# Kernel optimization log

Hardware: AMD Instinct MI355X
Metric: run time of the kernel (lower is better)

The kernel has to match this reference:

```python
import jax, jax.numpy as jnp
import numpy as np

NU = 50000   # num user nodes
NI = 50000   # num item nodes
E = 1600000  # edges per relation
DIN = 256    # in_features
H = 8        # n_heads
F = 64       # out_features per head (hidden = H*F = 512)
NEG_SLOPE = 0.2


def setup_inputs() -> dict:
    key = jax.random.key(0)
    ks = jax.random.split(key, 14)
    wscale = 0.05
    return {
        "x_user": jax.random.normal(ks[0], (NU, DIN), jnp.float32),
        "x_item": jax.random.normal(ks[1], (NI, DIN), jnp.float32),
        "Wv": jax.random.normal(ks[2], (3, DIN, H * F), jnp.float32) * wscale,
        "bv": jax.random.normal(ks[3], (3, H * F), jnp.float32) * wscale,
        "Wq": jax.random.normal(ks[4], (3, H * F, H), jnp.float32) * wscale,
        "bq": jax.random.normal(ks[5], (3, H), jnp.float32) * wscale,
        "Wk": jax.random.normal(ks[6], (3, H * F, H), jnp.float32) * wscale,
        "bk": jax.random.normal(ks[7], (3, H), jnp.float32) * wscale,
        "src1": jax.random.randint(ks[8], (E,), 0, NU, jnp.int32),   # user -> item
        "dst1": jax.random.randint(ks[9], (E,), 0, NI, jnp.int32),
        "src2": jax.random.randint(ks[10], (E,), 0, NI, jnp.int32),  # item -> user
        "dst2": jax.random.randint(ks[11], (E,), 0, NU, jnp.int32),
        "src3": jax.random.randint(ks[12], (E,), 0, NU, jnp.int32),  # user -> user
        "dst3": jax.random.randint(ks[13], (E,), 0, NU, jnp.int32),
    }


def _gat_relation(x_src, x_dst, Wv, bv, Wq, bq, Wk, bk, src, dst, n_dst):
    # linear_v on src and dst node features: [N, H*F]
    h_src = x_src @ Wv + bv
    h_dst = x_dst @ Wv + bv
    q = h_dst @ Wq + bq  # [Nd, H] per-head query logit
    k = h_src @ Wk + bk  # [Ns, H] per-head key logit
    # fused_gsddmm: gather to edges, leaky_relu, segment softmax over dst
    e = jax.nn.leaky_relu(q[dst] + k[src], NEG_SLOPE)  # [E, H]
    m = jax.ops.segment_max(e, dst, num_segments=n_dst)  # [Nd, H]
    m = jnp.where(jnp.isfinite(m), m, jnp.zeros_like(m))
    ex = jnp.exp(e - m[dst])
    denom = jax.ops.segment_sum(ex, dst, num_segments=n_dst)  # [Nd, H]
    attn = ex / jnp.maximum(denom[dst], 1e-9)  # [E, H]
    # gspmm: attention-weighted scatter-sum of src features into dst
    hs = h_src.reshape(-1, H, F)  # [Ns, H, F]
    agg = jax.ops.segment_sum(attn[:, :, None] * hs[src], dst, num_segments=n_dst)  # [Nd, H, F]
    return agg.mean(axis=1)  # torch.mean(h, dim=1) -> [Nd, F]


def reference(x_user, x_item, Wv, bv, Wq, bq, Wk, bk, src1, dst1, src2, dst2, src3, dst3):
    # relation 0: user -> item
    out_item = _gat_relation(x_user, x_item, Wv[0], bv[0], Wq[0], bq[0], Wk[0], bk[0], src1, dst1, NI)
    # relations 1 (item -> user) and 2 (user -> user) both target user: mean over relations
    r1 = _gat_relation(x_item, x_user, Wv[1], bv[1], Wq[1], bq[1], Wk[1], bk[1], src2, dst2, NU)
    r2 = _gat_relation(x_user, x_user, Wv[2], bv[2], Wq[2], bq[2], Wk[2], bk[2], src3, dst3, NU)
    out_user = (r1 + r2) / 2.0
    return out_user, out_item
```

## Files before the change

### kernel.cpp

```cpp
#include <hip/hip_runtime.h>

typedef unsigned short u16;
typedef __attribute__((ext_vector_type(4))) float f32x4;
typedef __attribute__((ext_vector_type(8))) short s16x8;

#define NND 50000
#define EDG 1600000
#define NBK 391
#define TOTB (3 * NBK)
#define TS 4096
#define CAPB 5120

__device__ __forceinline__ u16 f2b(float f) {
  union { float f; unsigned u; } c; c.f = f;
  unsigned r = c.u + 0x7fff + ((c.u >> 16) & 1);
  return (u16)(r >> 16);
}

__device__ __forceinline__ void accum8(float* num, uint4 u, float4 w0, float4 w1) {
  num[0] += w0.x * __int_as_float((int)(u.x << 16));
  num[1] += w0.y * __int_as_float((int)(u.x & 0xFFFF0000u));
  num[2] += w0.z * __int_as_float((int)(u.y << 16));
  num[3] += w0.w * __int_as_float((int)(u.y & 0xFFFF0000u));
  num[4] += w1.x * __int_as_float((int)(u.z << 16));
  num[5] += w1.y * __int_as_float((int)(u.z & 0xFFFF0000u));
  num[6] += w1.z * __int_as_float((int)(u.w << 16));
  num[7] += w1.w * __int_as_float((int)(u.w & 0xFFFF0000u));
}

__global__ void k_initcur(int* __restrict__ bcur) {
  int i = blockIdx.x * 256 + threadIdx.x;
  if (i < TOTB) bcur[i] = i * CAPB;
}

__global__ void k_prepw(const float* __restrict__ Wv, u16* __restrict__ Wt) {
  int tid = blockIdx.x * 256 + threadIdx.x;
  if (tid < 3 * 512 * 256) {
    int r = tid / (512 * 256); int rem = tid - r * 512 * 256;
    int n = rem >> 8; int kk = rem & 255;
    Wt[tid] = f2b(Wv[((size_t)r * 256 + kk) * 512 + n]);
  }
}

__global__ void k_fusew(const float* __restrict__ Wv, const float* __restrict__ bv,
                        const float* __restrict__ Wq, const float* __restrict__ bq,
                        const float* __restrict__ Wk, const float* __restrict__ bk,
                        float* __restrict__ FW, float* __restrict__ FB) {
  int tid = blockIdx.x * 256 + threadIdx.x;
  if (tid < 3 * 16 * 256) {
    int r = tid >> 12, o = (tid >> 8) & 15, kk = tid & 255;
    const float* wv = Wv + ((size_t)r * 256 + kk) * 512;
    const float* wqk = (o < 8) ? (Wq + r * 512 * 8 + o) : (Wk + r * 512 * 8 + (o - 8));
    float s = 0.f;
    for (int j = 0; j < 512; j++) s += wv[j] * wqk[j * 8];
    FW[tid] = s;
  }
  if (tid < 48) {
    int r = tid / 16, o = tid % 16;
    const float* wqk = (o < 8) ? (Wq + r * 512 * 8 + o) : (Wk + r * 512 * 8 + (o - 8));
    const float* bvp = bv + r * 512;
    float s = (o < 8) ? bq[r * 8 + o] : bk[r * 8 + (o - 8)];
    for (int j = 0; j < 512; j++) s += bvp[j] * wqk[j * 8];
    FB[tid] = s;
  }
}

__global__ void __launch_bounds__(256) kb_scatter(
    const int* __restrict__ s1, const int* __restrict__ d1,
    const int* __restrict__ s2, const int* __restrict__ d2,
    const int* __restrict__ s3, const int* __restrict__ d3,
    int* __restrict__ BCUR, unsigned* __restrict__ pairs) {
  __shared__ int h[NBK];
  __shared__ int bbase[NBK];
  int tid = threadIdx.x;
  int r = blockIdx.y;
  const int* dp = (r == 0) ? d1 : (r == 1) ? d2 : d3;
  const int* sp = (r == 0) ? s1 : (r == 1) ? s2 : s3;
  int e0 = blockIdx.x * TS;
  int n = EDG - e0; if (n > TS) n = TS;
  for (int b = tid; b < NBK; b += 256) h[b] = 0;
  __syncthreads();
  int eb[16]; unsigned ev[16];
#pragma unroll
  for (int k = 0; k < 16; k++) {
    int i = k * 256 + tid;
    if (i < n) {
      int d = dp[e0 + i], ss = sp[e0 + i];
      eb[k] = d >> 7;
      ev[k] = ((unsigned)(d & 127) << 16) | (unsigned)ss;
      atomicAdd(&h[eb[k]], 1);
    } else eb[k] = -1;
  }
  __syncthreads();
  for (int b = tid; b < NBK; b += 256) {
    int c = h[b];
    bbase[b] = c ? atomicAdd(&BCUR[r * NBK + b], c) : 0;
  }
  __syncthreads();
  for (int b = tid; b < NBK; b += 256) h[b] = 0;
  __syncthreads();
#pragma unroll
  for (int k = 0; k < 16; k++) {
    if (eb[k] >= 0) {
      int off = atomicAdd(&h[eb[k]], 1);
      int pos = bbase[eb[k]] + off;
      int limit = (r * NBK + eb[k] + 1) * CAPB;
      if (pos < limit) pairs[pos] = ev[k];
    }
  }
}

__global__ void __launch_bounds__(256) kb_build(
    const unsigned* __restrict__ pairs, const int* __restrict__ BCUR,
    int* __restrict__ rp, int* __restrict__ dgarr, int* __restrict__ csrc) {
  __shared__ int cntl[128];
  __shared__ int sc[128];
  __shared__ int curl[128];
  int t = threadIdx.x;
  int r = blockIdx.y, bx = blockIdx.x;
  int bin = r * NBK + bx;
  int base = bin * CAPB;
  int cnt = BCUR[bin] - base; if (cnt > CAPB) cnt = CAPB;
  int node0 = bx << 7;
  int nloc = NND - node0; if (nloc > 128) nloc = 128;
  if (t < 128) cntl[t] = 0;
  __syncthreads();
  for (int i = t; i < cnt; i += 256)
    atomicAdd(&cntl[pairs[base + i] >> 16], 1);
  __syncthreads();
  if (t < 128) sc[t] = cntl[t];
  __syncthreads();
  for (int off = 1; off < 128; off <<= 1) {
    int v = 0;
    if (t < 128) { v = sc[t]; if (t >= off) v += sc[t - off]; }
    __syncthreads();
    if (t < 128) sc[t] = v;
    __syncthreads();
  }
  if (t < 128) {
    int excl = sc[t] - cntl[t];
    if (t < nloc) { rp[r * NND + node0 + t] = base + excl; dgarr[r * NND + node0 + t] = cntl[t]; }
    curl[t] = base + excl;
  }
  __syncthreads();
  for (int i = t; i < cnt; i += 256) {
    unsigned v = pairs[base + i];
    int p = atomicAdd(&curl[v >> 16], 1);
    csrc[p] = (int)(v & 0xFFFFu);
  }
}

__global__ void __launch_bounds__(256) k_gemm(const float* __restrict__ A, const u16* __restrict__ Bt,
                                              const float* __restrict__ bias, u16* __restrict__ C, int M) {
  __shared__ u16 sA[128 * 72];
  __shared__ u16 sB[128 * 72];
  int tid = threadIdx.x;
  int lane = tid & 63, wid = tid >> 6;
  int wm = wid >> 1, wn = wid & 1;
  int l15 = lane & 15, l4 = lane >> 4;
  int m0 = blockIdx.x * 128, n0 = blockIdx.y * 128;
  f32x4 acc[4][4] = {};
  for (int ko = 0; ko < 256; ko += 64) {
#pragma unroll
    for (int p = 0; p < 4; p++) {
      int idx = p * 256 + tid;
      int row = idx >> 3, seg = idx & 7;
      int gm = m0 + row; if (gm >= M) gm = M - 1;
      float4 a0 = *(const float4*)(A + (size_t)gm * 256 + ko + seg * 8);
      float4 a1 = *(const float4*)(A + (size_t)gm * 256 + ko + seg * 8 + 4);
      s16x8 av;
      av[0] = (short)f2b(a0.x); av[1] = (short)f2b(a0.y);
      av[2] = (short)f2b(a0.z); av[3] = (short)f2b(a0.w);
      av[4] = (short)f2b(a1.x); av[5] = (short)f2b(a1.y);
      av[6] = (short)f2b(a1.z); av[7] = (short)f2b(a1.w);
      *(s16x8*)&sA[row * 72 + seg * 8] = av;
      *(s16x8*)&sB[row * 72 + seg * 8] = *(const s16x8*)(Bt + (n0 + row) * 256 + ko + seg * 8);
    }
    __syncthreads();
#pragma unroll
    for (int kk = 0; kk < 2; kk++) {
      s16x8 af[4], bf[4];
#pragma unroll
      for (int i = 0; i < 4; i++) af[i] = *(const s16x8*)&sA[(wm * 64 + i * 16 + l15) * 72 + kk * 32 + l4 * 8];
#pragma unroll
      for (int j = 0; j < 4; j++) bf[j] = *(const s16x8*)&sB[(wn * 64 + j * 16 + l15) * 72 + kk * 32 + l4 * 8];
#pragma unroll
      for (int i = 0; i < 4; i++)
#pragma unroll
        for (int j = 0; j < 4; j++)
          acc[i][j] = __builtin_amdgcn_mfma_f32_16x16x32_bf16(af[i], bf[j], acc[i][j], 0, 0, 0);
    }
    __syncthreads();
  }
#pragma unroll
  for (int j = 0; j < 4; j++) {
    int n = n0 + wn * 64 + j * 16 + l15;
    float bb = bias[n];
    int tpos = ((n & 63) << 3) + (n >> 6);
#pragma unroll
    for (int i = 0; i < 4; i++) {
      int mb = m0 + wm * 64 + i * 16 + l4 * 4;
#pragma unroll
      for (int r = 0; r < 4; r++) {
        int m = mb + r;
        if (m < M) C[(size_t)m * 512 + tpos] = f2b(acc[i][j][r] + bb);
      }
    }
  }
}

__global__ void __launch_bounds__(256) k_qk_u(
    const float* __restrict__ x, const float* __restrict__ FW,
    const float* __restrict__ FB, float* __restrict__ K0,
    float* __restrict__ Q1, float* __restrict__ Q2,
    float* __restrict__ K2, int N) {
  int lane = threadIdx.x & 63, wid = threadIdx.x >> 6;
  int stride = gridDim.x * 4;
  for (int row = blockIdx.x * 4 + wid; row < N; row += stride) {
    float4 xv = *(const float4*)(x + (size_t)row * 256 + lane * 4);
    {
      float p[16];
#pragma unroll
      for (int c = 0; c < 16; c++) {
        const float4 wv = *(const float4*)(FW + (size_t)(8 + c) * 256 + lane * 4);
        p[c] = xv.x * wv.x + xv.y * wv.y + xv.z * wv.z + xv.w * wv.w;
      }
#pragma unroll
      for (int off = 1; off < 64; off <<= 1)
#pragma unroll
        for (int c = 0; c < 16; c++) p[c] += __shfl_xor(p[c], off, 64);
      if (lane == 0) {
#pragma unroll
        for (int c = 0; c < 8; c++) K0[row * 8 + c] = p[c] + FB[8 + c];
#pragma unroll
        for (int c = 0; c < 8; c++) Q1[row * 8 + c] = p[8 + c] + FB[16 + c];
      }
    }
    {
      float p[16];
#pragma unroll
      for (int c = 0; c < 16; c++) {
        const float4 wv = *(const float4*)(FW + (size_t)(32 + c) * 256 + lane * 4);
        p[c] = xv.x * wv.x + xv.y * wv.y + xv.z * wv.z + xv.w * wv.w;
      }
#pragma unroll
      for (int off = 1; off < 64; off <<= 1)
#pragma unroll
        for (int c = 0; c < 16; c++) p[c] += __shfl_xor(p[c], off, 64);
      if (lane == 0) {
#pragma unroll
        for (int c = 0; c < 8; c++) Q2[row * 8 + c] = p[c] + FB[32 + c];
#pragma unroll
        for (int c = 0; c < 8; c++) K2[row * 8 + c] = p[8 + c] + FB[40 + c];
      }
    }
  }
}

__global__ void __launch_bounds__(256) k_qk_i(
    const float* __restrict__ x, const float* __restrict__ FW,
    const float* __restrict__ FB, float* __restrict__ Q0,
    float* __restrict__ K1, int N) {
  int lane = threadIdx.x & 63, wid = threadIdx.x >> 6;
  int stride = gridDim.x * 4;
  for (int row = blockIdx.x * 4 + wid; row < N; row += stride) {
    float4 xv = *(const float4*)(x + (size_t)row * 256 + lane * 4);
    float p[16];
#pragma unroll
    for (int c = 0; c < 16; c++) {
      const float4 wv = *(const float4*)(FW + (size_t)((c < 8) ? c : (16 + c)) * 256 + lane * 4);
      p[c] = xv.x * wv.x + xv.y * wv.y + xv.z * wv.z + xv.w * wv.w;
    }
#pragma unroll
    for (int off = 1; off < 64; off <<= 1)
#pragma unroll
      for (int c = 0; c < 16; c++) p[c] += __shfl_xor(p[c], off, 64);
    if (lane == 0) {
#pragma unroll
      for (int c = 0; c < 8; c++) Q0[row * 8 + c] = p[c] + FB[c];
#pragma unroll
      for (int c = 0; c < 8; c++) K1[row * 8 + c] = p[8 + c] + FB[24 + c];
    }
  }
}

__global__ void __launch_bounds__(256) k_edge(
    const int* __restrict__ rp, const int* __restrict__ dg, const int* __restrict__ csrc,
    const float* __restrict__ q, const float* __restrict__ k,
    const u16* __restrict__ hs, float* __restrict__ out,
    float scale, int accum) {
  __shared__ float exw[4][64 * 8];
  __shared__ int sarr[4][64];
  __shared__ float sd[4][8];
  __shared__ float sacc[4][64];
  int lane = threadIdx.x & 63, w = threadIdx.x >> 6;
  int dst = blockIdx.x * 2 + (w >> 1);
  int half = w & 1;
  int beg = rp[dst];
  int deg = dg[dst];
  int hlen = (deg + 1) >> 1;
  int s0 = half ? hlen : 0;
  int s1 = half ? deg : hlen;
  float qv[8];
  {
    float4 q0 = *(const float4*)(q + dst * 8);
    float4 q1 = *(const float4*)(q + dst * 8 + 4);
    qv[0] = q0.x; qv[1] = q0.y; qv[2] = q0.z; qv[3] = q0.w;
    qv[4] = q1.x; qv[5] = q1.y; qv[6] = q1.z; qv[7] = q1.w;
  }
  float num[8] = {0, 0, 0, 0, 0, 0, 0, 0};
  float dsum[8] = {0, 0, 0, 0, 0, 0, 0, 0};
  for (int base = s0; base < s1; base += 64) {
    int i = base + lane;
    int nn = min(64, s1 - base);
    if (i < s1) {
      int s = csrc[beg + i];
      sarr[w][lane] = s;
      float4 k0 = *(const float4*)(k + s * 8);
      float4 k1 = *(const float4*)(k + s * 8 + 4);
      float kv[8] = {k0.x, k0.y, k0.z, k0.w, k1.x, k1.y, k1.z, k1.w};
#pragma unroll
      for (int h = 0; h < 8; h++) {
        float e = qv[h] + kv[h];
        e = e > 0.f ? e : 0.2f * e;
        float wgt = exp2f(e * 1.44269504f);
        exw[w][lane * 8 + h] = wgt;
        dsum[h] += wgt;
      }
    }
    __asm__ __volatile__("s_waitcnt lgkmcnt(0)" ::: "memory");
    int j = 0;
    for (; j + 4 <= nn; j += 4) {
      int sa = sarr[w][j], sb = sarr[w][j + 1], sc = sarr[w][j + 2], sdn = sarr[w][j + 3];
      uint4 ua = *(const uint4*)(hs + (size_t)sa * 512 + lane * 8);
      uint4 ub = *(const uint4*)(hs + (size_t)sb * 512 + lane * 8);
      uint4 uc = *(const uint4*)(hs + (size_t)sc * 512 + lane * 8);
      uint4 ud = *(const uint4*)(hs + (size_t)sdn * 512 + lane * 8);
      float4 wa0 = *(const float4*)&exw[w][j * 8],       wa1 = *(const float4*)&exw[w][j * 8 + 4];
      float4 wb0 = *(const float4*)&exw[w][j * 8 + 8],   wb1 = *(const float4*)&exw[w][j * 8 + 12];
      float4 wc0 = *(const float4*)&exw[w][j * 8 + 16],  wc1 = *(const float4*)&exw[w][j * 8 + 20];
      float4 wd0 = *(const float4*)&exw[w][j * 8 + 24],  wd1 = *(const float4*)&exw[w][j * 8 + 28];
      accum8(num, ua, wa0, wa1);
      accum8(num, ub, wb0, wb1);
      accum8(num, uc, wc0, wc1);
      accum8(num, ud, wd0, wd1);
    }
    for (; j < nn; j++) {
      int s = sarr[w][j];
      uint4 u = *(const uint4*)(hs + (size_t)s * 512 + lane * 8);
      float4 e0 = *(const float4*)&exw[w][j * 8];
      float4 e1 = *(const float4*)&exw[w][j * 8 + 4];
      accum8(num, u, e0, e1);
    }
  }
#pragma unroll
  for (int off = 1; off < 64; off <<= 1)
#pragma unroll
    for (int h = 0; h < 8; h++) dsum[h] += __shfl_xor(dsum[h], off, 64);
  if (lane == 0) {
#pragma unroll
    for (int h = 0; h < 8; h++) sd[w][h] = dsum[h];
  }
  __syncthreads();
  float acc = 0.f;
#pragma unroll
  for (int h = 0; h < 8; h++) {
    float tot = sd[w][h] + sd[w ^ 1][h];
    float rden = tot > 0.f ? 1.f / tot : 0.f;
    acc += num[h] * rden;
  }
  acc *= scale;
  sacc[w][lane] = acc;
  __syncthreads();
  if (half == 0) {
    float tot = sacc[w][lane] + sacc[w + 1][lane];
    if (accum) out[dst * 64 + lane] += tot;
    else out[dst * 64 + lane] = tot;
  }
}

extern "C" void kernel_launch(void* const* d_in, const int* in_sizes, int n_in,
                              void* d_out, int out_size, void* d_ws, size_t ws_size,
                              hipStream_t stream) {
  const float* xu = (const float*)d_in[0];
  const float* xi = (const float*)d_in[1];
  const float* Wv = (const float*)d_in[2];
  const float* bv = (const float*)d_in[3];
  const float* Wq = (const float*)d_in[4];
  const float* bq = (const float*)d_in[5];
  const float* Wk = (const float*)d_in[6];
  const float* bk = (const float*)d_in[7];
  const int* src1 = (const int*)d_in[8];
  const int* dst1 = (const int*)d_in[9];
  const int* src2 = (const int*)d_in[10];
  const int* dst2 = (const int*)d_in[11];
  const int* src3 = (const int*)d_in[12];
  const int* dst3 = (const int*)d_in[13];
  float* out_user = (float*)d_out;
  float* out_item = out_user + (size_t)NND * 64;

  char* w = (char*)d_ws;
  auto alloc = [&](size_t sz) -> char* {
    char* p = w; w += (sz + 255) & ~(size_t)255; return p;
  };
  u16* H    = (u16*)alloc((size_t)NND * 512 * 2);
  u16* WT   = (u16*)alloc((size_t)3 * 512 * 256 * 2);
  float* FW = (float*)alloc((size_t)3 * 16 * 256 * 4);
  float* FB = (float*)alloc((size_t)3 * 16 * 4);
  float* Q0 = (float*)alloc((size_t)NND * 8 * 4);
  float* K0 = (float*)alloc((size_t)NND * 8 * 4);
  float* Q1 = (float*)alloc((size_t)NND * 8 * 4);
  float* K1 = (float*)alloc((size_t)NND * 8 * 4);
  float* Q2 = (float*)alloc((size_t)NND * 8 * 4);
  float* K2 = (float*)alloc((size_t)NND * 8 * 4);
  int* ROWPTR = (int*)alloc((size_t)3 * NND * 4);
  int* DEG    = (int*)alloc((size_t)3 * NND * 4);
  int* BCUR   = (int*)alloc(TOTB * 4);
  int* CSRC   = (int*)alloc((size_t)TOTB * CAPB * 4);
  unsigned* PAIRS = (unsigned*)H;
  (void)ws_size; (void)n_in; (void)in_sizes; (void)out_size;

  k_initcur<<<(TOTB + 255) / 256, 256, 0, stream>>>(BCUR);
  kb_scatter<<<dim3((EDG + TS - 1) / TS, 3), 256, 0, stream>>>(src1, dst1, src2, dst2, src3, dst3, BCUR, PAIRS);
  kb_build<<<dim3(NBK, 3), 256, 0, stream>>>(PAIRS, BCUR, ROWPTR, DEG, CSRC);

  k_prepw<<<(3 * 512 * 256 + 255) / 256, 256, 0, stream>>>(Wv, WT);
  k_fusew<<<48, 256, 0, stream>>>(Wv, bv, Wq, bq, Wk, bk, FW, FB);

  k_qk_u<<<1024, 256, 0, stream>>>(xu, FW, FB, K0, Q1, Q2, K2, NND);
  k_qk_i<<<1024, 256, 0, stream>>>(xi, FW, FB, Q0, K1, NND);

  dim3 gg((NND + 127) / 128, 4);
  k_gemm<<<gg, 256, 0, stream>>>(xu, WT,                 bv,        H, NND);
  k_edge<<<NND / 2, 256, 0, stream>>>(ROWPTR,           DEG,           CSRC, Q0, K0, H, out_item, 0.125f,  0);
  k_gemm<<<gg, 256, 0, stream>>>(xi, WT + 512 * 256,     bv + 512,  H, NND);
  k_edge<<<NND / 2, 256, 0, stream>>>(ROWPTR + NND,     DEG + NND,     CSRC, Q1, K1, H, out_user, 0.0625f, 0);
  k_gemm<<<gg, 256, 0, stream>>>(xu, WT + 2 * 512 * 256, bv + 1024, H, NND);
  k_edge<<<NND / 2, 256, 0, stream>>>(ROWPTR + 2 * NND, DEG + 2 * NND, CSRC, Q2, K2, H, out_user, 0.0625f, 1);
}
```

Measured before the change: 1.218 ms.

## Merge setup kernels, coalesce weight-fusion, and store CSR sources as 16-bit

Folds the bucket-cursor init into the weight-prep kernel and merges the user and item QK projection kernels into one launch, removing several small launches. The Wv·Wq/Wk fusion now reads a transposed fp32 copy of Wv, so each thread's loads are coalesced and the bias term is computed with a block reduction instead of long serial per-thread loops. CSR source indices are stored as u16 rather than int, which halves the index memory traffic in the build and edge kernels. The extra fp32 transposed weight buffer costs workspace and an additional write, and 16-bit indices depend on node counts staying below 65536.

```diff
diff --git a/kernel.cpp b/kernel.cpp
--- a/kernel.cpp
+++ b/kernel.cpp
@@ -28,40 +28,44 @@
   num[7] += w1.w * __int_as_float((int)(u.w & 0xFFFF0000u));
 }
 
-__global__ void k_initcur(int* __restrict__ bcur) {
-  int i = blockIdx.x * 256 + threadIdx.x;
-  if (i < TOTB) bcur[i] = i * CAPB;
-}
-
-__global__ void k_prepw(const float* __restrict__ Wv, u16* __restrict__ Wt) {
+__global__ void k_prepw(const float* __restrict__ Wv, u16* __restrict__ Wt,
+                        float* __restrict__ Wvt, int* __restrict__ bcur) {
   int tid = blockIdx.x * 256 + threadIdx.x;
   if (tid < 3 * 512 * 256) {
     int r = tid / (512 * 256); int rem = tid - r * 512 * 256;
     int n = rem >> 8; int kk = rem & 255;
-    Wt[tid] = f2b(Wv[((size_t)r * 256 + kk) * 512 + n]);
-  }
-}
-
-__global__ void k_fusew(const float* __restrict__ Wv, const float* __restrict__ bv,
-                        const float* __restrict__ Wq, const float* __restrict__ bq,
-                        const float* __restrict__ Wk, const float* __restrict__ bk,
-                        float* __restrict__ FW, float* __restrict__ FB) {
-  int tid = blockIdx.x * 256 + threadIdx.x;
-  if (tid < 3 * 16 * 256) {
-    int r = tid >> 12, o = (tid >> 8) & 15, kk = tid & 255;
-    const float* wv = Wv + ((size_t)r * 256 + kk) * 512;
-    const float* wqk = (o < 8) ? (Wq + r * 512 * 8 + o) : (Wk + r * 512 * 8 + (o - 8));
-    float s = 0.f;
-    for (int j = 0; j < 512; j++) s += wv[j] * wqk[j * 8];
-    FW[tid] = s;
-  }
-  if (tid < 48) {
-    int r = tid / 16, o = tid % 16;
-    const float* wqk = (o < 8) ? (Wq + r * 512 * 8 + o) : (Wk + r * 512 * 8 + (o - 8));
-    const float* bvp = bv + r * 512;
-    float s = (o < 8) ? bq[r * 8 + o] : bk[r * 8 + (o - 8)];
-    for (int j = 0; j < 512; j++) s += bvp[j] * wqk[j * 8];
-    FB[tid] = s;
+    float v = Wv[((size_t)r * 256 + kk) * 512 + n];
+    Wt[tid] = f2b(v);
+    Wvt[tid] = v;
+  }
+  if (tid < TOTB) bcur[tid] = tid * CAPB;
+}
+
+__global__ void __launch_bounds__(256) k_fusew2(
+    const float* __restrict__ Wvt, const float* __restrict__ bv,
+    const float* __restrict__ Wq, const float* __restrict__ bq,
+    const float* __restrict__ Wk, const float* __restrict__ bk,
+    float* __restrict__ FW, float* __restrict__ FB) {
+  __shared__ float red[256];
+  int r = blockIdx.x >> 4, o = blockIdx.x & 15;
+  int t = threadIdx.x;
+  const float* wvt = Wvt + (size_t)r * 512 * 256;
+  const float* wqk = (o < 8) ? (Wq + (size_t)r * 512 * 8 + o) : (Wk + (size_t)r * 512 * 8 + (o - 8));
+  float acc = 0.f;
+#pragma unroll 8
+  for (int j = 0; j < 512; j++) acc += wvt[(size_t)j * 256 + t] * wqk[j * 8];
+  FW[((size_t)r * 16 + o) * 256 + t] = acc;
+  float pb = 0.f;
+  for (int j = t; j < 512; j += 256) pb += bv[r * 512 + j] * wqk[j * 8];
+  red[t] = pb;
+  __syncthreads();
+  for (int off = 128; off > 0; off >>= 1) {
+    if (t < off) red[t] += red[t + off];
+    __syncthreads();
+  }
+  if (t == 0) {
+    float b = (o < 8) ? bq[r * 8 + o] : bk[r * 8 + (o - 8)];
+    FB[r * 16 + o] = red[0] + b;
   }
 }
 
@@ -112,7 +116,7 @@
 
 __global__ void __launch_bounds__(256) kb_build(
     const unsigned* __restrict__ pairs, const int* __restrict__ BCUR,
-    int* __restrict__ rp, int* __restrict__ dgarr, int* __restrict__ csrc) {
+    int* __restrict__ rp, int* __restrict__ dgarr, u16* __restrict__ csrc) {
   __shared__ int cntl[128];
   __shared__ int sc[128];
   __shared__ int curl[128];
@@ -146,7 +150,7 @@
   for (int i = t; i < cnt; i += 256) {
     unsigned v = pairs[base + i];
     int p = atomicAdd(&curl[v >> 16], 1);
-    csrc[p] = (int)(v & 0xFFFFu);
+    csrc[p] = (u16)(v & 0xFFFFu);
   }
 }
 
@@ -209,20 +213,62 @@
   }
 }
 
-__global__ void __launch_bounds__(256) k_qk_u(
-    const float* __restrict__ x, const float* __restrict__ FW,
-    const float* __restrict__ FB, float* __restrict__ K0,
-    float* __restrict__ Q1, float* __restrict__ Q2,
-    float* __restrict__ K2, int N) {
+__global__ void __launch_bounds__(256) k_qk(
+    const float* __restrict__ xu, const float* __restrict__ xi,
+    const float* __restrict__ FW, const float* __restrict__ FB,
+    float* __restrict__ K0, float* __restrict__ Q1, float* __restrict__ Q2,
+    float* __restrict__ K2, float* __restrict__ Q0, float* __restrict__ K1) {
   int lane = threadIdx.x & 63, wid = threadIdx.x >> 6;
-  int stride = gridDim.x * 4;
-  for (int row = blockIdx.x * 4 + wid; row < N; row += stride) {
-    float4 xv = *(const float4*)(x + (size_t)row * 256 + lane * 4);
-    {
+  if (blockIdx.x < 1024) {
+    int stride = 1024 * 4;
+    for (int row = blockIdx.x * 4 + wid; row < NND; row += stride) {
+      float4 xv = *(const float4*)(xu + (size_t)row * 256 + lane * 4);
+      {
+        float p[16];
+#pragma unroll
+        for (int c = 0; c < 16; c++) {
+          const float4 wv = *(const float4*)(FW + (size_t)(8 + c) * 256 + lane * 4);
+          p[c] = xv.x * wv.x + xv.y * wv.y + xv.z * wv.z + xv.w * wv.w;
+        }
+#pragma unroll
+        for (int off = 1; off < 64; off <<= 1)
+#pragma unroll
+          for (int c = 0; c < 16; c++) p[c] += __shfl_xor(p[c], off, 64);
+        if (lane == 0) {
+#pragma unroll
+          for (int c = 0; c < 8; c++) K0[row * 8 + c] = p[c] + FB[8 + c];
+#pragma unroll
+          for (int c = 0; c < 8; c++) Q1[row * 8 + c] = p[8 + c] + FB[16 + c];
+        }
+      }
+      {
+        float p[16];
+#pragma unroll
+        for (int c = 0; c < 16; c++) {
+          const float4 wv = *(const float4*)(FW + (size_t)(32 + c) * 256 + lane * 4);
+          p[c] = xv.x * wv.x + xv.y * wv.y + xv.z * wv.z + xv.w * wv.w;
+        }
+#pragma unroll
+        for (int off = 1; off < 64; off <<= 1)
+#pragma unroll
+          for (int c = 0; c < 16; c++) p[c] += __shfl_xor(p[c], off, 64);
+        if (lane == 0) {
+#pragma unroll
+          for (int c = 0; c < 8; c++) Q2[row * 8 + c] = p[c] + FB[32 + c];
+#pragma unroll
+          for (int c = 0; c < 8; c++) K2[row * 8 + c] = p[8 + c] + FB[40 + c];
+        }
+      }
+    }
+  } else {
+    int b = blockIdx.x - 1024;
+    int stride = 512 * 4;
+    for (int row = b * 4 + wid; row < NND; row += stride) {
+      float4 xv = *(const float4*)(xi + (size_t)row * 256 + lane * 4);
       float p[16];
 #pragma unroll
       for (int c = 0; c < 16; c++) {
-        const float4 wv = *(const float4*)(FW + (size_t)(8 + c) * 256 + lane * 4);
+        const float4 wv = *(const float4*)(FW + (size_t)((c < 8) ? c : (16 + c)) * 256 + lane * 4);
         p[c] = xv.x * wv.x + xv.y * wv.y + xv.z * wv.z + xv.w * wv.w;
       }
 #pragma unroll
@@ -231,61 +277,16 @@
         for (int c = 0; c < 16; c++) p[c] += __shfl_xor(p[c], off, 64);
       if (lane == 0) {
 #pragma unroll
-        for (int c = 0; c < 8; c++) K0[row * 8 + c] = p[c] + FB[8 + c];
-#pragma unroll
-        for (int c = 0; c < 8; c++) Q1[row * 8 + c] = p[8 + c] + FB[16 + c];
-      }
-    }
-    {
-      float p[16];
-#pragma unroll
-      for (int c = 0; c < 16; c++) {
-        const float4 wv = *(const float4*)(FW + (size_t)(32 + c) * 256 + lane * 4);
-        p[c] = xv.x * wv.x + xv.y * wv.y + xv.z * wv.z + xv.w * wv.w;
-      }
-#pragma unroll
-      for (int off = 1; off < 64; off <<= 1)
-#pragma unroll
-        for (int c = 0; c < 16; c++) p[c] += __shfl_xor(p[c], off, 64);
-      if (lane == 0) {
-#pragma unroll
-        for (int c = 0; c < 8; c++) Q2[row * 8 + c] = p[c] + FB[32 + c];
-#pragma unroll
-        for (int c = 0; c < 8; c++) K2[row * 8 + c] = p[8 + c] + FB[40 + c];
-      }
-    }
-  }
-}
-
-__global__ void __launch_bounds__(256) k_qk_i(
-    const float* __restrict__ x, const float* __restrict__ FW,
-    const float* __restrict__ FB, float* __restrict__ Q0,
-    float* __restrict__ K1, int N) {
-  int lane = threadIdx.x & 63, wid = threadIdx.x >> 6;
-  int stride = gridDim.x * 4;
-  for (int row = blockIdx.x * 4 + wid; row < N; row += stride) {
-    float4 xv = *(const float4*)(x + (size_t)row * 256 + lane * 4);
-    float p[16];
-#pragma unroll
-    for (int c = 0; c < 16; c++) {
-      const float4 wv = *(const float4*)(FW + (size_t)((c < 8) ? c : (16 + c)) * 256 + lane * 4);
-      p[c] = xv.x * wv.x + xv.y * wv.y + xv.z * wv.z + xv.w * wv.w;
-    }
-#pragma unroll
-    for (int off = 1; off < 64; off <<= 1)
-#pragma unroll
-      for (int c = 0; c < 16; c++) p[c] += __shfl_xor(p[c], off, 64);
-    if (lane == 0) {
-#pragma unroll
-      for (int c = 0; c < 8; c++) Q0[row * 8 + c] = p[c] + FB[c];
-#pragma unroll
-      for (int c = 0; c < 8; c++) K1[row * 8 + c] = p[8 + c] + FB[24 + c];
+        for (int c = 0; c < 8; c++) Q0[row * 8 + c] = p[c] + FB[c];
+#pragma unroll
+        for (int c = 0; c < 8; c++) K1[row * 8 + c] = p[8 + c] + FB[24 + c];
+      }
     }
   }
 }
 
 __global__ void __launch_bounds__(256) k_edge(
-    const int* __restrict__ rp, const int* __restrict__ dg, const int* __restrict__ csrc,
+    const int* __restrict__ rp, const int* __restrict__ dg, const u16* __restrict__ csrc,
     const float* __restrict__ q, const float* __restrict__ k,
     const u16* __restrict__ hs, float* __restrict__ out,
     float scale, int accum) {
@@ -314,7 +315,7 @@
     int i = base + lane;
     int nn = min(64, s1 - base);
     if (i < s1) {
-      int s = csrc[beg + i];
+      int s = (int)csrc[beg + i];
       sarr[w][lane] = s;
       float4 k0 = *(const float4*)(k + s * 8);
       float4 k1 = *(const float4*)(k + s * 8 + 4);
@@ -403,10 +404,11 @@
   auto alloc = [&](size_t sz) -> char* {
     char* p = w; w += (sz + 255) & ~(size_t)255; return p;
   };
-  u16* H    = (u16*)alloc((size_t)NND * 512 * 2);
-  u16* WT   = (u16*)alloc((size_t)3 * 512 * 256 * 2);
-  float* FW = (float*)alloc((size_t)3 * 16 * 256 * 4);
-  float* FB = (float*)alloc((size_t)3 * 16 * 4);
+  u16* H     = (u16*)alloc((size_t)NND * 512 * 2);
+  u16* WT    = (u16*)alloc((size_t)3 * 512 * 256 * 2);
+  float* WVT = (float*)alloc((size_t)3 * 512 * 256 * 4);
+  float* FW  = (float*)alloc((size_t)3 * 16 * 256 * 4);
+  float* FB  = (float*)alloc((size_t)3 * 16 * 4);
   float* Q0 = (float*)alloc((size_t)NND * 8 * 4);
   float* K0 = (float*)alloc((size_t)NND * 8 * 4);
   float* Q1 = (float*)alloc((size_t)NND * 8 * 4);
@@ -416,19 +418,17 @@
   int* ROWPTR = (int*)alloc((size_t)3 * NND * 4);
   int* DEG    = (int*)alloc((size_t)3 * NND * 4);
   int* BCUR   = (int*)alloc(TOTB * 4);
-  int* CSRC   = (int*)alloc((size_t)TOTB * CAPB * 4);
+  u16* CSRC   = (u16*)alloc((size_t)TOTB * CAPB * 2);
   unsigned* PAIRS = (unsigned*)H;
   (void)ws_size; (void)n_in; (void)in_sizes; (void)out_size;
 
-  k_initcur<<<(TOTB + 255) / 256, 256, 0, stream>>>(BCUR);
+  k_prepw<<<(3 * 512 * 256 + 255) / 256, 256, 0, stream>>>(Wv, WT, WVT, BCUR);
+
   kb_scatter<<<dim3((EDG + TS - 1) / TS, 3), 256, 0, stream>>>(src1, dst1, src2, dst2, src3, dst3, BCUR, PAIRS);
   kb_build<<<dim3(NBK, 3), 256, 0, stream>>>(PAIRS, BCUR, ROWPTR, DEG, CSRC);
 
-  k_prepw<<<(3 * 512 * 256 + 255) / 256, 256, 0, stream>>>(Wv, WT);
-  k_fusew<<<48, 256, 0, stream>>>(Wv, bv, Wq, bq, Wk, bk, FW, FB);
-
-  k_qk_u<<<1024, 256, 0, stream>>>(xu, FW, FB, K0, Q1, Q2, K2, NND);
-  k_qk_i<<<1024, 256, 0, stream>>>(xi, FW, FB, Q0, K1, NND);
+  k_fusew2<<<48, 256, 0, stream>>>(WVT, bv, Wq, bq, Wk, bk, FW, FB);
+  k_qk<<<1536, 256, 0, stream>>>(xu, xi, FW, FB, K0, Q1, Q2, K2, Q0, K1);
 
   dim3 gg((NND + 127) / 128, 4);
   k_gemm<<<gg, 256, 0, stream>>>(xu, WT,                 bv,        H, NND);
```

New measurement: 1.209 ms. About the same (-0.8%).
